# Performance work log

Measured on AMD Instinct MI355X. Metric: run time of the kernel, lower is better.

The kernel has to match this reference:

```python
import jax, jax.numpy as jnp
import numpy as np

N = 50000
E = 800000
IN_DIM = 128
HID = 128
OUT = 40


def setup_inputs() -> dict:
    key = jax.random.key(0)
    k1, k2, k3, k4, k5 = jax.random.split(key, 5)
    x = jax.random.normal(k1, (N, IN_DIM), dtype=jnp.float32)
    edge_index = jax.random.randint(k2, (2, E), 0, N, dtype=jnp.int64)
    # Glorot-ish init for GCNConv weights, zero bias (PyG default bias=True)
    W1 = jax.random.normal(k3, (IN_DIM, HID), dtype=jnp.float32) / np.sqrt(IN_DIM)
    b1 = jnp.zeros((HID,), dtype=jnp.float32)
    W2 = jax.random.normal(k4, (HID, OUT), dtype=jnp.float32) / np.sqrt(HID)
    b2 = jnp.zeros((OUT,), dtype=jnp.float32)
    return {"x": x, "edge_index": edge_index, "W1": W1, "b1": b1, "W2": W2, "b2": b2}


def _gcn_norm(edge_index, n_nodes):
    """Add self-loops and compute symmetric GCN normalization per edge.
    Returns (src, dst, norm) with len E + n_nodes."""
    loops = jnp.arange(n_nodes, dtype=edge_index.dtype)
    src = jnp.concatenate([edge_index[0], loops])
    dst = jnpp_concat = jnp.concatenate([edge_index[1], loops])
    dst = jnp.concatenate([edge_index[1], loops])
    deg = jax.ops.segment_sum(jnp.ones_like(dst, dtype=jnp.float32), dst,
                              num_segments=n_nodes)
    dinv = jnp.where(deg > 0, jax.lax.rsqrt(deg), 0.0)
    norm = dinv[src] * dinv[dst]  # [E + N]
    return src, dst, norm


def _gcn_conv(x, src, dst, norm, W, b, n_nodes):
    xw = x @ W                                  # [N, F_out] transform first
    msg = xw[src] * norm[:, None]               # gather + scale, [E+N, F_out]
    out = jax.ops.segment_sum(msg, dst, num_segments=n_nodes)  # scatter-add
    return out + b


def reference(x, edge_index, W1, b1, W2, b2):
    n = x.shape[0]
    src, dst, norm = _gcn_norm(edge_index, n)
    h = _gcn_conv(x, src, dst, norm, W1, b1, n)
    h = jax.nn.relu(h)
    # dropout is identity in eval mode (training=False)
    h = _gcn_conv(h, src, dst, norm, W2, b2, n)
    return jax.nn.softmax(h, axis=1)
```

## Files before the change

### kernel.cpp

```cpp
#include <hip/hip_runtime.h>
#include <hip/hip_fp16.h>

#define IN_DIM 128
#define HID    128
#define OUTC   40
#define CAP    64
#define LSTR   136
#define NBS    1024
#define NBG1   256

typedef _Float16 f16x8 __attribute__((ext_vector_type(8)));
typedef _Float16 f16x4 __attribute__((ext_vector_type(4)));
typedef float    f32x4 __attribute__((ext_vector_type(4)));
typedef int      i32x4 __attribute__((ext_vector_type(4)));

__device__ __forceinline__ int permi(int d, int NP8) { return (d & 7) * NP8 + (d >> 3); }

__device__ __forceinline__ f16x8 cvt8(f32x4 lo, f32x4 hi) {
  f16x8 r;
  r[0] = (_Float16)lo[0]; r[1] = (_Float16)lo[1]; r[2] = (_Float16)lo[2]; r[3] = (_Float16)lo[3];
  r[4] = (_Float16)hi[0]; r[5] = (_Float16)hi[1]; r[6] = (_Float16)hi[2]; r[7] = (_Float16)hi[3];
  return r;
}

__global__ __launch_bounds__(256) void k_scatter_gemm1(const int* __restrict__ edge, int* __restrict__ cnt,
                                                       unsigned short* __restrict__ col,
                                                       const float* __restrict__ x, const float* __restrict__ W1,
                                                       __half* __restrict__ xws,
                                                       int E, int n, int NP8, int nT) {
  __shared__ _Float16 sW[128 * LSTR];
  int b   = blockIdx.x;
  int c40 = b / 40, r40 = b % 40;

  if (r40 < 32) {
    int g = b & 7;
    auto proc = [&](int d, int s) {
      if ((d & 7) != g || (unsigned)d >= (unsigned)n || (unsigned)s >= (unsigned)n) return;
      int p   = g * NP8 + (d >> 3);
      int pos = atomicAdd(&cnt[p], 1);
      if (pos < CAP) col[(size_t)p * CAP + pos] = (unsigned short)s;
    };
    int j = c40 * 4 + (r40 >> 3);
    int t = j * 256 + threadIdx.x;
    const int gstride = (NBS >> 3) * 256;
    int E4 = E >> 2;
    const i32x4* srcv = (const i32x4*)edge;
    const i32x4* dstv = (const i32x4*)&edge[E];
    for (int q = t; q < E4; q += gstride) {
      i32x4 dq = __builtin_nontemporal_load(&dstv[q]);
      i32x4 sq = __builtin_nontemporal_load(&srcv[q]);
      proc(dq[0], sq[0]); proc(dq[1], sq[1]); proc(dq[2], sq[2]); proc(dq[3], sq[3]);
    }
    if (b == 0) {
      for (int e = E4 * 4 + threadIdx.x; e < E; e += 256) {
        int d  = edge[E + e];
        int sv = edge[e];
        if ((unsigned)d >= (unsigned)n || (unsigned)sv >= (unsigned)n) continue;
        int p   = (d & 7) * NP8 + (d >> 3);
        int pos = atomicAdd(&cnt[p], 1);
        if (pos < CAP) col[(size_t)p * CAP + pos] = (unsigned short)sv;
      }
    }
    return;
  }

  int tid = threadIdx.x;
  {
    const f32x4* w4 = (const f32x4*)W1;
    for (int idx = tid; idx < 4096; idx += 256) {
      int kk = idx >> 5, nn4 = (idx & 31) * 4;
      f32x4 v = w4[idx];
      sW[(nn4 + 0) * LSTR + kk] = (_Float16)v[0];
      sW[(nn4 + 1) * LSTR + kk] = (_Float16)v[1];
      sW[(nn4 + 2) * LSTR + kk] = (_Float16)v[2];
      sW[(nn4 + 3) * LSTR + kk] = (_Float16)v[3];
    }
  }
  __syncthreads();
  int wv = tid >> 6, lane = tid & 63, m = lane & 15, quad = lane >> 4;
  int bg = c40 * 8 + (r40 - 32);
  for (int tile = bg; tile < nT; tile += NBG1) {
    int i0   = tile * 64;
    int arow = i0 + 16 * wv + m;
    f16x8 a0, a1, a2, a3;
    if (arow < n) {
      const float* xr = &x[(size_t)arow * IN_DIM + quad * 8];
      f32x4 u0 = __builtin_nontemporal_load((const f32x4*)(xr));
      f32x4 u1 = __builtin_nontemporal_load((const f32x4*)(xr + 4));
      f32x4 u2 = __builtin_nontemporal_load((const f32x4*)(xr + 32));
      f32x4 u3 = __builtin_nontemporal_load((const f32x4*)(xr + 36));
      f32x4 u4 = __builtin_nontemporal_load((const f32x4*)(xr + 64));
      f32x4 u5 = __builtin_nontemporal_load((const f32x4*)(xr + 68));
      f32x4 u6 = __builtin_nontemporal_load((const f32x4*)(xr + 96));
      f32x4 u7 = __builtin_nontemporal_load((const f32x4*)(xr + 100));
      a0 = cvt8(u0, u1); a1 = cvt8(u2, u3); a2 = cvt8(u4, u5); a3 = cvt8(u6, u7);
    } else {
#pragma unroll
      for (int jj = 0; jj < 8; ++jj) {
        a0[jj] = (_Float16)0.f; a1[jj] = (_Float16)0.f; a2[jj] = (_Float16)0.f; a3[jj] = (_Float16)0.f;
      }
    }
    int base_row = i0 + 16 * wv + quad * 4;
#pragma unroll
    for (int t = 0; t < 8; ++t) {
      const _Float16* bx = &sW[(t * 16 + m) * LSTR + quad * 8];
      f16x8 bf0 = *(const f16x8*)(bx);
      f16x8 bf1 = *(const f16x8*)(bx + 32);
      f16x8 bf2 = *(const f16x8*)(bx + 64);
      f16x8 bf3 = *(const f16x8*)(bx + 96);
      f32x4 c = {0.f, 0.f, 0.f, 0.f};
      c = __builtin_amdgcn_mfma_f32_16x16x32_f16(a0, bf0, c, 0, 0, 0);
      c = __builtin_amdgcn_mfma_f32_16x16x32_f16(a1, bf1, c, 0, 0, 0);
      c = __builtin_amdgcn_mfma_f32_16x16x32_f16(a2, bf2, c, 0, 0, 0);
      c = __builtin_amdgcn_mfma_f32_16x16x32_f16(a3, bf3, c, 0, 0, 0);
      int colb = t * 16 + m;
#pragma unroll
      for (int r = 0; r < 4; ++r) {
        int row = base_row + r;
        if (row < n) xws[(size_t)row * HID + colb] = __float2half(c[r]);
      }
    }
  }
}

__global__ __launch_bounds__(256) void k_agg1_gemm2(const uint2* __restrict__ xws2, const int* __restrict__ cnt,
                                                    const unsigned short* __restrict__ col,
                                                    const float* __restrict__ b1, const float* __restrict__ W2,
                                                    __half* __restrict__ hw, int n, int NP8) {
  __shared__ _Float16 sW[48 * LSTR];
  __shared__ _Float16 sH[64 * LSTR];
  int tid = threadIdx.x;
  int i0  = blockIdx.x * 64;

  for (int idx = tid; idx < 8192; idx += 256) {
    int nn = idx & 63, kk = idx >> 6;
    if (nn < 48) sW[nn * LSTR + kk] = (nn < OUTC) ? (_Float16)W2[kk * OUTC + nn] : (_Float16)0.f;
  }

  int hwid = tid >> 5, f = tid & 31;
  float4 bb = ((const float4*)b1)[f];
#pragma unroll 1
  for (int it = 0; it < 8; ++it) {
    int r   = it * 8 + hwid;
    int row = i0 + r;
    float ax = 0.f, ay = 0.f, az = 0.f, aw = 0.f;
    if (row < n) {
      int p     = permi(row, NP8);
      int deg   = cnt[p];
      float dvd = rsqrtf((float)(deg + 1));
      uint2 sv  = xws2[(size_t)row * 32 + f];
      float2 slo = __half22float2(*(__half2*)&sv.x);
      float2 shi = __half22float2(*(__half2*)&sv.y);
      ax = slo.x * dvd; ay = slo.y * dvd; az = shi.x * dvd; aw = shi.y * dvd;
      int end = min(deg, CAP);
      const unsigned short* cp = &col[(size_t)p * CAP];
      int e = 0;
      for (; e + 4 <= end; e += 4) {
        int s0 = cp[e], s1 = cp[e + 1], s2 = cp[e + 2], s3 = cp[e + 3];
        float d0 = rsqrtf((float)(cnt[permi(s0, NP8)] + 1));
        float d1 = rsqrtf((float)(cnt[permi(s1, NP8)] + 1));
        float d2 = rsqrtf((float)(cnt[permi(s2, NP8)] + 1));
        float d3 = rsqrtf((float)(cnt[permi(s3, NP8)] + 1));
        uint2 v0 = xws2[(size_t)s0 * 32 + f];
        uint2 v1 = xws2[(size_t)s1 * 32 + f];
        uint2 v2 = xws2[(size_t)s2 * 32 + f];
        uint2 v3 = xws2[(size_t)s3 * 32 + f];
        float2 l0 = __half22float2(*(__half2*)&v0.x), h0 = __half22float2(*(__half2*)&v0.y);
        float2 l1 = __half22float2(*(__half2*)&v1.x), h1 = __half22float2(*(__half2*)&v1.y);
        float2 l2 = __half22float2(*(__half2*)&v2.x), h2 = __half22float2(*(__half2*)&v2.y);
        float2 l3 = __half22float2(*(__half2*)&v3.x), h3 = __half22float2(*(__half2*)&v3.y);
        ax += l0.x * d0 + l1.x * d1 + l2.x * d2 + l3.x * d3;
        ay += l0.y * d0 + l1.y * d1 + l2.y * d2 + l3.y * d3;
        az += h0.x * d0 + h1.x * d1 + h2.x * d2 + h3.x * d3;
        aw += h0.y * d0 + h1.y * d1 + h2.y * d2 + h3.y * d3;
      }
      for (; e < end; ++e) {
        int s    = cp[e];
        float dv = rsqrtf((float)(cnt[permi(s, NP8)] + 1));
        uint2 v  = xws2[(size_t)s * 32 + f];
        float2 l = __half22float2(*(__half2*)&v.x), hh = __half22float2(*(__half2*)&v.y);
        ax += l.x * dv; ay += l.y * dv; az += hh.x * dv; aw += hh.y * dv;
      }
      ax = fmaxf(ax * dvd + bb.x, 0.f);
      ay = fmaxf(ay * dvd + bb.y, 0.f);
      az = fmaxf(az * dvd + bb.z, 0.f);
      aw = fmaxf(aw * dvd + bb.w, 0.f);
    }
    f16x4 hv4;
    hv4[0] = (_Float16)ax; hv4[1] = (_Float16)ay; hv4[2] = (_Float16)az; hv4[3] = (_Float16)aw;
    *(f16x4*)&sH[r * LSTR + f * 4] = hv4;
  }
  __syncthreads();

  int wv = tid >> 6, lane = tid & 63, m = lane & 15, quad = lane >> 4;
  const _Float16* axp = &sH[(16 * wv + m) * LSTR + quad * 8];
  f16x8 a0 = *(const f16x8*)(axp);
  f16x8 a1 = *(const f16x8*)(axp + 32);
  f16x8 a2 = *(const f16x8*)(axp + 64);
  f16x8 a3 = *(const f16x8*)(axp + 96);

  int base_row = i0 + 16 * wv + quad * 4;
  float dvr[4];
#pragma unroll
  for (int r = 0; r < 4; ++r) {
    int row = base_row + r;
    dvr[r] = (row < n) ? rsqrtf((float)(cnt[permi(row, NP8)] + 1)) : 0.f;
  }

#pragma unroll
  for (int t = 0; t < 3; ++t) {
    const _Float16* bx = &sW[(t * 16 + m) * LSTR + quad * 8];
    f16x8 bf0 = *(const f16x8*)(bx);
    f16x8 bf1 = *(const f16x8*)(bx + 32);
    f16x8 bf2 = *(const f16x8*)(bx + 64);
    f16x8 bf3 = *(const f16x8*)(bx + 96);
    f32x4 c = {0.f, 0.f, 0.f, 0.f};
    c = __builtin_amdgcn_mfma_f32_16x16x32_f16(a0, bf0, c, 0, 0, 0);
    c = __builtin_amdgcn_mfma_f32_16x16x32_f16(a1, bf1, c, 0, 0, 0);
    c = __builtin_amdgcn_mfma_f32_16x16x32_f16(a2, bf2, c, 0, 0, 0);
    c = __builtin_amdgcn_mfma_f32_16x16x32_f16(a3, bf3, c, 0, 0, 0);
    int colb = t * 16 + m;
    if (colb < OUTC) {
#pragma unroll
      for (int r = 0; r < 4; ++r) {
        int row = base_row + r;
        if (row < n) hw[(size_t)row * OUTC + colb] = __float2half(c[r] * dvr[r]);
      }
    }
  }
}

__global__ __launch_bounds__(256) void k_agg2(const __half2* __restrict__ hw2, const int* __restrict__ cnt,
                                              const unsigned short* __restrict__ col, const float* __restrict__ b2,
                                              float* __restrict__ out, int n, int NP8) {
  int wpair = (blockIdx.x * 256 + threadIdx.x) >> 6;
  int lane  = threadIdx.x & 63;
  int half  = lane >> 5;
  int f     = lane & 31;
  int wid   = wpair * 2 + half;
  bool act  = (f < OUTC / 2) && (wid < n);
  int widc  = (wid < n) ? wid : 0;
  int li    = act ? f : 0;
  int p     = permi(widc, NP8);
  int deg   = (wid < n) ? cnt[p] : 0;
  float2 acc = act ? __half22float2(hw2[(size_t)widc * (OUTC / 2) + li]) : make_float2(0.f, 0.f);
  int end = min(deg, CAP);
  const unsigned short* cp = &col[(size_t)p * CAP];
  int e = 0;
  for (; e + 8 <= end; e += 8) {
    int s0 = cp[e], s1 = cp[e+1], s2 = cp[e+2], s3 = cp[e+3];
    int s4 = cp[e+4], s5 = cp[e+5], s6 = cp[e+6], s7 = cp[e+7];
    if (act) {
      float2 v0 = __half22float2(hw2[(size_t)s0 * (OUTC / 2) + li]);
      float2 v1 = __half22float2(hw2[(size_t)s1 * (OUTC / 2) + li]);
      float2 v2 = __half22float2(hw2[(size_t)s2 * (OUTC / 2) + li]);
      float2 v3 = __half22float2(hw2[(size_t)s3 * (OUTC / 2) + li]);
      float2 v4 = __half22float2(hw2[(size_t)s4 * (OUTC / 2) + li]);
      float2 v5 = __half22float2(hw2[(size_t)s5 * (OUTC / 2) + li]);
      float2 v6 = __half22float2(hw2[(size_t)s6 * (OUTC / 2) + li]);
      float2 v7 = __half22float2(hw2[(size_t)s7 * (OUTC / 2) + li]);
      acc.x += (v0.x + v1.x) + (v2.x + v3.x) + ((v4.x + v5.x) + (v6.x + v7.x));
      acc.y += (v0.y + v1.y) + (v2.y + v3.y) + ((v4.y + v5.y) + (v6.y + v7.y));
    }
  }
  for (; e < end; ++e) {
    int s = cp[e];
    if (act) {
      float2 v = __half22float2(hw2[(size_t)s * (OUTC / 2) + li]);
      acc.x += v.x; acc.y += v.y;
    }
  }
  float dvd = rsqrtf((float)(deg + 1));
  float2 bb = act ? ((const float2*)b2)[li] : make_float2(0.f, 0.f);
  float lx = act ? acc.x * dvd + bb.x : -1e30f;
  float ly = act ? acc.y * dvd + bb.y : -1e30f;
  float m = fmaxf(lx, ly);
#pragma unroll
  for (int o = 16; o > 0; o >>= 1) m = fmaxf(m, __shfl_xor(m, o, 32));
  float ex = act ? __expf(lx - m) : 0.f;
  float ey = act ? __expf(ly - m) : 0.f;
  float sum = ex + ey;
#pragma unroll
  for (int o = 16; o > 0; o >>= 1) sum += __shfl_xor(sum, o, 32);
  if (act) {
    float inv = 1.f / sum;
    ((float2*)out)[(size_t)wid * (OUTC / 2) + li] = make_float2(ex * inv, ey * inv);
  }
}


extern "C" void kernel_launch(void* const* d_in, const int* in_sizes, int n_in,
                              void* d_out, int out_size, void* d_ws, size_t ws_size,
                              hipStream_t stream) {
  const float* x    = (const float*)d_in[0];
  const int*   edge = (const int*)d_in[1];
  const float* W1   = (const float*)d_in[2];
  const float* b1   = (const float*)d_in[3];
  const float* W2   = (const float*)d_in[4];
  const float* b2   = (const float*)d_in[5];
  float* out = (float*)d_out;

  int N   = in_sizes[0] / IN_DIM;
  int E   = in_sizes[1] / 2;
  int NP8 = (N + 7) / 8;
  int NP  = NP8 * 8;

  char* ws = (char*)d_ws;
  size_t off = 0;
  auto carve = [&](size_t bytes) { char* p = ws + off; off = (off + bytes + 255) & ~(size_t)255; return p; };
  int*            cnt = (int*)carve((size_t)NP * 4);
  unsigned short* col = (unsigned short*)carve((size_t)NP * CAP * 2);
  __half*         xws = (__half*)carve((size_t)N * HID * 2);
  __half*         hw  = (__half*)carve((size_t)N * OUTC * 2);

  (void)hipMemsetAsync(cnt, 0, (size_t)NP * 4, stream);

  int nT   = (N + 63) / 64;
  int nbA2 = ((N + 1) / 2 * 64 + 255) / 256;

  k_scatter_gemm1<<<NBS + NBG1, 256, 0, stream>>>(edge, cnt, col, x, W1, xws, E, N, NP8, nT);
  k_agg1_gemm2<<<nT, 256, 0, stream>>>((const uint2*)xws, cnt, col, b1, W2, hw, N, NP8);
  k_agg2<<<nbA2, 256, 0, stream>>>((const __half2*)hw, cnt, col, b2, out, N, NP8);
}
```

Measured before the change: 230.2 us.

## Split fused aggregation+GEMM2 into separate kernels and swizzle W1 LDS layout

The fused layer-1 aggregation plus GEMM2 kernel is split into a standalone aggregation kernel with one half-wave per node, writing relu'd hidden features to a new fp16 buffer, and a separate GEMM2 kernel that loads those rows into LDS. The aim is higher parallelism and latency hiding in the gather-bound aggregation, which the old design limited by running 64 rows per block serially. The W1 shared-memory tile moves from a padded stride to an XOR-swizzled layout, and the neighbour-index lists are read with vector loads. In exchange it adds an extra kernel launch and a full N x 128 fp16 round trip through global memory.

```diff
diff --git a/kernel.cpp b/kernel.cpp
--- a/kernel.cpp
+++ b/kernel.cpp
@@ -28,9 +28,11 @@
                                                        const float* __restrict__ x, const float* __restrict__ W1,
                                                        __half* __restrict__ xws,
                                                        int E, int n, int NP8, int nT) {
-  __shared__ _Float16 sW[128 * LSTR];
+  __shared__ _Float16 sW[128 * 128];
   int b   = blockIdx.x;
   int c40 = b / 40, r40 = b % 40;
+  int tid = threadIdx.x;
+  int E4  = E >> 2;
 
   if (r40 < 32) {
     int g = b & 7;
@@ -41,9 +43,8 @@
       if (pos < CAP) col[(size_t)p * CAP + pos] = (unsigned short)s;
     };
     int j = c40 * 4 + (r40 >> 3);
-    int t = j * 256 + threadIdx.x;
+    int t = j * 256 + tid;
     const int gstride = (NBS >> 3) * 256;
-    int E4 = E >> 2;
     const i32x4* srcv = (const i32x4*)edge;
     const i32x4* dstv = (const i32x4*)&edge[E];
     for (int q = t; q < E4; q += gstride) {
@@ -52,7 +53,7 @@
       proc(dq[0], sq[0]); proc(dq[1], sq[1]); proc(dq[2], sq[2]); proc(dq[3], sq[3]);
     }
     if (b == 0) {
-      for (int e = E4 * 4 + threadIdx.x; e < E; e += 256) {
+      for (int e = E4 * 4 + tid; e < E; e += 256) {
         int d  = edge[E + e];
         int sv = edge[e];
         if ((unsigned)d >= (unsigned)n || (unsigned)sv >= (unsigned)n) continue;
@@ -64,20 +65,21 @@
     return;
   }
 
-  int tid = threadIdx.x;
   {
     const f32x4* w4 = (const f32x4*)W1;
     for (int idx = tid; idx < 4096; idx += 256) {
       int kk = idx >> 5, nn4 = (idx & 31) * 4;
       f32x4 v = w4[idx];
-      sW[(nn4 + 0) * LSTR + kk] = (_Float16)v[0];
-      sW[(nn4 + 1) * LSTR + kk] = (_Float16)v[1];
-      sW[(nn4 + 2) * LSTR + kk] = (_Float16)v[2];
-      sW[(nn4 + 3) * LSTR + kk] = (_Float16)v[3];
+#pragma unroll
+      for (int j = 0; j < 4; ++j) {
+        int nn = nn4 + j;
+        sW[nn * 128 + (kk ^ ((nn & 7) << 3))] = (_Float16)v[j];
+      }
     }
   }
   __syncthreads();
   int wv = tid >> 6, lane = tid & 63, m = lane & 15, quad = lane >> 4;
+  int sw = (m & 7) << 3;
   int bg = c40 * 8 + (r40 - 32);
   for (int tile = bg; tile < nT; tile += NBG1) {
     int i0   = tile * 64;
@@ -103,11 +105,11 @@
     int base_row = i0 + 16 * wv + quad * 4;
 #pragma unroll
     for (int t = 0; t < 8; ++t) {
-      const _Float16* bx = &sW[(t * 16 + m) * LSTR + quad * 8];
-      f16x8 bf0 = *(const f16x8*)(bx);
-      f16x8 bf1 = *(const f16x8*)(bx + 32);
-      f16x8 bf2 = *(const f16x8*)(bx + 64);
-      f16x8 bf3 = *(const f16x8*)(bx + 96);
+      const _Float16* bx = &sW[(t * 16 + m) * 128];
+      f16x8 bf0 = *(const f16x8*)&bx[(quad * 8 +  0) ^ sw];
+      f16x8 bf1 = *(const f16x8*)&bx[(quad * 8 + 32) ^ sw];
+      f16x8 bf2 = *(const f16x8*)&bx[(quad * 8 + 64) ^ sw];
+      f16x8 bf3 = *(const f16x8*)&bx[(quad * 8 + 96) ^ sw];
       f32x4 c = {0.f, 0.f, 0.f, 0.f};
       c = __builtin_amdgcn_mfma_f32_16x16x32_f16(a0, bf0, c, 0, 0, 0);
       c = __builtin_amdgcn_mfma_f32_16x16x32_f16(a1, bf1, c, 0, 0, 0);
@@ -123,10 +125,63 @@
   }
 }
 
-__global__ __launch_bounds__(256) void k_agg1_gemm2(const uint2* __restrict__ xws2, const int* __restrict__ cnt,
-                                                    const unsigned short* __restrict__ col,
-                                                    const float* __restrict__ b1, const float* __restrict__ W2,
-                                                    __half* __restrict__ hw, int n, int NP8) {
+__global__ __launch_bounds__(256) void k_agg1(const uint2* __restrict__ xws2, const int* __restrict__ cnt,
+                                              const unsigned short* __restrict__ col, const float* __restrict__ b1,
+                                              uint2* __restrict__ hv, int n, int NP8) {
+  int wvid = (blockIdx.x * 256 + threadIdx.x) >> 6;
+  int lane = threadIdx.x & 63;
+  int half = lane >> 5;
+  int f    = lane & 31;
+  int wid  = wvid * 2 + half;
+  if (wid >= n) return;
+  int p   = permi(wid, NP8);
+  int deg = cnt[p];
+  float dvd = rsqrtf((float)(deg + 1));
+  uint2 sv = xws2[(size_t)wid * 32 + f];
+  float2 slo = __half22float2(*(__half2*)&sv.x);
+  float2 shi = __half22float2(*(__half2*)&sv.y);
+  float ax = slo.x * dvd, ay = slo.y * dvd, az = shi.x * dvd, aw = shi.y * dvd;
+  int end = min(deg, CAP);
+  const unsigned short* cp = &col[(size_t)p * CAP];
+  int e = 0;
+  for (; e + 4 <= end; e += 4) {
+    uint2 cw = *(const uint2*)&cp[e];
+    int s0 = cw.x & 0xffff, s1 = cw.x >> 16;
+    int s2 = cw.y & 0xffff, s3 = cw.y >> 16;
+    float d0 = rsqrtf((float)(cnt[permi(s0, NP8)] + 1));
+    float d1 = rsqrtf((float)(cnt[permi(s1, NP8)] + 1));
+    float d2 = rsqrtf((float)(cnt[permi(s2, NP8)] + 1));
+    float d3 = rsqrtf((float)(cnt[permi(s3, NP8)] + 1));
+    uint2 v0 = xws2[(size_t)s0 * 32 + f];
+    uint2 v1 = xws2[(size_t)s1 * 32 + f];
+    uint2 v2 = xws2[(size_t)s2 * 32 + f];
+    uint2 v3 = xws2[(size_t)s3 * 32 + f];
+    float2 l0 = __half22float2(*(__half2*)&v0.x), h0 = __half22float2(*(__half2*)&v0.y);
+    float2 l1 = __half22float2(*(__half2*)&v1.x), h1 = __half22float2(*(__half2*)&v1.y);
+    float2 l2 = __half22float2(*(__half2*)&v2.x), h2 = __half22float2(*(__half2*)&v2.y);
+    float2 l3 = __half22float2(*(__half2*)&v3.x), h3 = __half22float2(*(__half2*)&v3.y);
+    ax += l0.x * d0 + l1.x * d1 + l2.x * d2 + l3.x * d3;
+    ay += l0.y * d0 + l1.y * d1 + l2.y * d2 + l3.y * d3;
+    az += h0.x * d0 + h1.x * d1 + h2.x * d2 + h3.x * d3;
+    aw += h0.y * d0 + h1.y * d1 + h2.y * d2 + h3.y * d3;
+  }
+  for (; e < end; ++e) {
+    int s    = cp[e];
+    float dv = rsqrtf((float)(cnt[permi(s, NP8)] + 1));
+    uint2 v  = xws2[(size_t)s * 32 + f];
+    float2 l = __half22float2(*(__half2*)&v.x), hh = __half22float2(*(__half2*)&v.y);
+    ax += l.x * dv; ay += l.y * dv; az += hh.x * dv; aw += hh.y * dv;
+  }
+  float4 bb = ((const float4*)b1)[f];
+  __half2 o0 = __floats2half2_rn(fmaxf(ax * dvd + bb.x, 0.f), fmaxf(ay * dvd + bb.y, 0.f));
+  __half2 o1 = __floats2half2_rn(fmaxf(az * dvd + bb.z, 0.f), fmaxf(aw * dvd + bb.w, 0.f));
+  uint2 o; o.x = *(unsigned*)&o0; o.y = *(unsigned*)&o1;
+  hv[(size_t)wid * 32 + f] = o;
+}
+
+__global__ __launch_bounds__(256) void k_gemm2(const __half* __restrict__ h, const float* __restrict__ W2,
+                                               const int* __restrict__ cnt, __half* __restrict__ out,
+                                               int n, int NP8) {
   __shared__ _Float16 sW[48 * LSTR];
   __shared__ _Float16 sH[64 * LSTR];
   int tid = threadIdx.x;
@@ -136,59 +191,14 @@
     int nn = idx & 63, kk = idx >> 6;
     if (nn < 48) sW[nn * LSTR + kk] = (nn < OUTC) ? (_Float16)W2[kk * OUTC + nn] : (_Float16)0.f;
   }
-
-  int hwid = tid >> 5, f = tid & 31;
-  float4 bb = ((const float4*)b1)[f];
-#pragma unroll 1
-  for (int it = 0; it < 8; ++it) {
-    int r   = it * 8 + hwid;
-    int row = i0 + r;
-    float ax = 0.f, ay = 0.f, az = 0.f, aw = 0.f;
-    if (row < n) {
-      int p     = permi(row, NP8);
-      int deg   = cnt[p];
-      float dvd = rsqrtf((float)(deg + 1));
-      uint2 sv  = xws2[(size_t)row * 32 + f];
-      float2 slo = __half22float2(*(__half2*)&sv.x);
-      float2 shi = __half22float2(*(__half2*)&sv.y);
-      ax = slo.x * dvd; ay = slo.y * dvd; az = shi.x * dvd; aw = shi.y * dvd;
-      int end = min(deg, CAP);
-      const unsigned short* cp = &col[(size_t)p * CAP];
-      int e = 0;
-      for (; e + 4 <= end; e += 4) {
-        int s0 = cp[e], s1 = cp[e + 1], s2 = cp[e + 2], s3 = cp[e + 3];
-        float d0 = rsqrtf((float)(cnt[permi(s0, NP8)] + 1));
-        float d1 = rsqrtf((float)(cnt[permi(s1, NP8)] + 1));
-        float d2 = rsqrtf((float)(cnt[permi(s2, NP8)] + 1));
-        float d3 = rsqrtf((float)(cnt[permi(s3, NP8)] + 1));
-        uint2 v0 = xws2[(size_t)s0 * 32 + f];
-        uint2 v1 = xws2[(size_t)s1 * 32 + f];
-        uint2 v2 = xws2[(size_t)s2 * 32 + f];
-        uint2 v3 = xws2[(size_t)s3 * 32 + f];
-        float2 l0 = __half22float2(*(__half2*)&v0.x), h0 = __half22float2(*(__half2*)&v0.y);
-        float2 l1 = __half22float2(*(__half2*)&v1.x), h1 = __half22float2(*(__half2*)&v1.y);
-        float2 l2 = __half22float2(*(__half2*)&v2.x), h2 = __half22float2(*(__half2*)&v2.y);
-        float2 l3 = __half22float2(*(__half2*)&v3.x), h3 = __half22float2(*(__half2*)&v3.y);
-        ax += l0.x * d0 + l1.x * d1 + l2.x * d2 + l3.x * d3;
-        ay += l0.y * d0 + l1.y * d1 + l2.y * d2 + l3.y * d3;
-        az += h0.x * d0 + h1.x * d1 + h2.x * d2 + h3.x * d3;
-        aw += h0.y * d0 + h1.y * d1 + h2.y * d2 + h3.y * d3;
-      }
-      for (; e < end; ++e) {
-        int s    = cp[e];
-        float dv = rsqrtf((float)(cnt[permi(s, NP8)] + 1));
-        uint2 v  = xws2[(size_t)s * 32 + f];
-        float2 l = __half22float2(*(__half2*)&v.x), hh = __half22float2(*(__half2*)&v.y);
-        ax += l.x * dv; ay += l.y * dv; az += hh.x * dv; aw += hh.y * dv;
-      }
-      ax = fmaxf(ax * dvd + bb.x, 0.f);
-      ay = fmaxf(ay * dvd + bb.y, 0.f);
-      az = fmaxf(az * dvd + bb.z, 0.f);
-      aw = fmaxf(aw * dvd + bb.w, 0.f);
-    }
-    f16x4 hv4;
-    hv4[0] = (_Float16)ax; hv4[1] = (_Float16)ay; hv4[2] = (_Float16)az; hv4[3] = (_Float16)aw;
-    *(f16x4*)&sH[r * LSTR + f * 4] = hv4;
+  {
+    const uint4* src = (const uint4*)h;
+    for (int idx = tid; idx < 1024; idx += 256) {
+      int r = idx >> 4, c = idx & 15;
+      int row = i0 + r;
+      uint4 v = (row < n) ? src[(size_t)row * 16 + c] : make_uint4(0u, 0u, 0u, 0u);
+      *(uint4*)&sH[r * LSTR + c * 8] = v;
+    }
   }
   __syncthreads();
 
@@ -224,7 +234,7 @@
 #pragma unroll
       for (int r = 0; r < 4; ++r) {
         int row = base_row + r;
-        if (row < n) hw[(size_t)row * OUTC + colb] = __float2half(c[r] * dvr[r]);
+        if (row < n) out[(size_t)row * OUTC + colb] = __float2half(c[r] * dvr[r]);
       }
     }
   }
@@ -248,8 +258,9 @@
   const unsigned short* cp = &col[(size_t)p * CAP];
   int e = 0;
   for (; e + 8 <= end; e += 8) {
-    int s0 = cp[e], s1 = cp[e+1], s2 = cp[e+2], s3 = cp[e+3];
-    int s4 = cp[e+4], s5 = cp[e+5], s6 = cp[e+6], s7 = cp[e+7];
+    uint4 cw = *(const uint4*)&cp[e];
+    int s0 = cw.x & 0xffff, s1 = cw.x >> 16, s2 = cw.y & 0xffff, s3 = cw.y >> 16;
+    int s4 = cw.z & 0xffff, s5 = cw.z >> 16, s6 = cw.w & 0xffff, s7 = cw.w >> 16;
     if (act) {
       float2 v0 = __half22float2(hw2[(size_t)s0 * (OUTC / 2) + li]);
       float2 v1 = __half22float2(hw2[(size_t)s1 * (OUTC / 2) + li]);
@@ -311,14 +322,16 @@
   int*            cnt = (int*)carve((size_t)NP * 4);
   unsigned short* col = (unsigned short*)carve((size_t)NP * CAP * 2);
   __half*         xws = (__half*)carve((size_t)N * HID * 2);
-  __half*         hw  = (__half*)carve((size_t)N * OUTC * 2);
+  __half*         h   = (__half*)carve((size_t)N * HID * 2);
+  __half*         hw  = xws;
 
   (void)hipMemsetAsync(cnt, 0, (size_t)NP * 4, stream);
 
-  int nT   = (N + 63) / 64;
-  int nbA2 = ((N + 1) / 2 * 64 + 255) / 256;
+  int nT  = (N + 63) / 64;
+  int nbA = ((N + 1) / 2 * 64 + 255) / 256;
 
   k_scatter_gemm1<<<NBS + NBG1, 256, 0, stream>>>(edge, cnt, col, x, W1, xws, E, N, NP8, nT);
-  k_agg1_gemm2<<<nT, 256, 0, stream>>>((const uint2*)xws, cnt, col, b1, W2, hw, N, NP8);
-  k_agg2<<<nbA2, 256, 0, stream>>>((const __half2*)hw, cnt, col, b2, out, N, NP8);
-}
+  k_agg1<<<nbA, 256, 0, stream>>>((const uint2*)xws, cnt, col, b1, (uint2*)h, N, NP8);
+  k_gemm2<<<nT, 256, 0, stream>>>(h, W2, cnt, hw, N, NP8);
+  k_agg2<<<nbA, 256, 0, stream>>>((const __half2*)hw, cnt, col, b2, out, N, NP8);
+}
```

New measurement: 212.6 us. 1.08x faster.
